# Kernel tuning notes

Measured on AMD Instinct MI355X. Metric: run time of the kernel, lower is better.

Reference implementation:

```python
import jax, jax.numpy as jnp
import numpy as np

B, T_MEL, T_TXT = 16, 2048, 1024
D_MODEL, D_ENC_M, D_ENC_T = 512, 512, 512
LN_EPS = 1e-5


def setup_inputs() -> dict:
    key = jax.random.key(0)
    ks = jax.random.split(key, 9)
    mel_encoding = jax.random.normal(ks[0], (B, T_MEL, D_ENC_M), dtype=jnp.float32)
    text_encoding = jax.random.normal(ks[1], (B, T_TXT, D_ENC_T), dtype=jnp.float32)
    mel_mask = jax.random.randint(ks[2], (B, T_MEL), 0, 2).astype(bool)
    mel_mask = mel_mask.at[:, 0].set(False)  # guarantee >=1 unmasked key per row
    src_mask = jax.random.randint(ks[3], (B, T_TXT), 0, 2).astype(bool)
    # Projection weights stored [in, out] (torch Linear does x @ W.T)
    sc = 1.0 / np.sqrt(D_ENC_M)
    Wq = jax.random.uniform(ks[4], (D_ENC_T, D_MODEL), jnp.float32, -sc, sc)
    Wk = jax.random.uniform(ks[5], (D_ENC_M, D_MODEL), jnp.float32, -sc, sc)
    Wv = jax.random.uniform(ks[6], (D_ENC_M, D_MODEL), jnp.float32, -sc, sc)
    ln_gamma = jnp.ones((D_MODEL,), jnp.float32)
    ln_beta = jnp.zeros((D_MODEL,), jnp.float32)
    return {"mel_encoding": mel_encoding, "text_encoding": text_encoding,
            "mel_mask": mel_mask, "src_mask": src_mask,
            "Wq": Wq, "Wk": Wk, "Wv": Wv,
            "ln_gamma": ln_gamma, "ln_beta": ln_beta}


def reference(mel_encoding, text_encoding, mel_mask, src_mask, Wq, Wk, Wv, ln_gamma, ln_beta):
    temperature = jnp.sqrt(jnp.float32(D_ENC_M))
    q = jnp.einsum('btd,dm->btm', text_encoding, Wq)   # [B, T_txt, d_model]
    k = jnp.einsum('bsd,dm->bsm', mel_encoding, Wk)    # [B, T_mel, d_model]
    v = jnp.einsum('bsd,dm->bsm', mel_encoding, Wv)
    # attn_mask = outer product of src_mask and mel_mask (True -> masked)
    attn_mask = src_mask[:, :, None] & mel_mask[:, None, :]  # [B, T_txt, T_mel]
    scores = jnp.einsum('btm,bsm->bts', q, k) / temperature
    scores = jnp.where(attn_mask, -jnp.inf, scores)
    attn = jax.nn.softmax(scores, axis=2)
    output = jnp.einsum('bts,bsm->btm', attn, v)
    # dropout is identity at inference; LayerNorm over last dim
    mean = jnp.mean(output, axis=-1, keepdims=True)
    var = jnp.var(output, axis=-1, keepdims=True)
    output = (output - mean) * jax.lax.rsqrt(var + LN_EPS) * ln_gamma + ln_beta
    return output, attn
```

## Files before the change

### kernel.cpp

```cpp
#include <hip/hip_runtime.h>

#define DEV __device__ __forceinline__

typedef __attribute__((ext_vector_type(8))) short short8v;
typedef __attribute__((ext_vector_type(4))) float f32x4;

DEV unsigned short f2bf(float f) {
  unsigned int x = __float_as_uint(f);
  x = x + 0x7FFFu + ((x >> 16) & 1u);
  return (unsigned short)(x >> 16);
}
DEV float bf2f(unsigned short u) {
  return __uint_as_float(((unsigned)u) << 16);
}

DEV int swz_byte(int row, int kElem) {
  int chunk = ((kElem >> 3) ^ (row & 7));
  return row * 128 + (chunk << 4) + ((kElem & 7) << 1);
}

template <int ROUNDS>
DEV void stage(const unsigned short* __restrict__ g, int ld,
               unsigned short* tile, int tid) {
  const int wave = tid >> 6, l = tid & 63;
#pragma unroll
  for (int p = 0; p < ROUNDS; ++p) {
    const int r = (p << 5) + (wave << 3) + (l >> 3);
    const int c = ((l & 7) ^ (r & 7)) << 3;
    const unsigned short* src = g + (long)r * ld + c;
#if __has_builtin(__builtin_amdgcn_global_load_lds)
    unsigned short* dst = tile + (p << 11) + (wave << 9);
    __builtin_amdgcn_global_load_lds(
        (const __attribute__((address_space(1))) void*)src,
        (__attribute__((address_space(3))) void*)dst, 16, 0, 0);
#else
    short8v v = *reinterpret_cast<const short8v*>(src);
    *reinterpret_cast<short8v*>(reinterpret_cast<char*>(tile) +
                                (p << 12) + (wave << 10) + (l << 4)) = v;
#endif
  }
}

template <int BM>
DEV void stage_f32(const float* __restrict__ g, int ld,
                   unsigned short* tile, int tid) {
  const int rl = tid >> 4;
  const int c4 = (tid & 15) << 2;
#pragma unroll
  for (int p = 0; p < BM / 16; ++p) {
    const int row = (p << 4) + rl;
    const float4 f = *reinterpret_cast<const float4*>(g + (long)row * ld + c4);
    ushort4 pack;
    pack.x = f2bf(f.x); pack.y = f2bf(f.y); pack.z = f2bf(f.z); pack.w = f2bf(f.w);
    *reinterpret_cast<ushort4*>(reinterpret_cast<char*>(tile) +
                                swz_byte(row, c4)) = pack;
  }
}

template <int BM, int EPI, int GM, bool AF32>
__global__ __launch_bounds__(256) void gemm_bf16(
    const void* __restrict__ Av, const unsigned short* __restrict__ B,
    void* __restrict__ Cout, int M, int N, int K,
    long aBatch, long bBatch, long cBatch,
    const int* __restrict__ srcMask, const int* __restrict__ melMask,
    float scale, float* __restrict__ stats) {
  constexpr int NI = BM / 32;
  __shared__ unsigned short As[BM * 64];
  __shared__ unsigned short Bs[128 * 64];
  const int tid = threadIdx.x;
  const int lane = tid & 63;
  const int wave = tid >> 6;
  int z, bmi, bni;
  if constexpr (GM == 1) {
    const int id = blockIdx.x;
    z = (id & 7) | ((id >> 10) << 3);
    const int ib = (id >> 3) & 127;
    bni = ib & 15;
    bmi = ib >> 4;
  } else if constexpr (GM == 2) {
    bmi = blockIdx.x; bni = blockIdx.y; z = blockIdx.z;
  } else {
    bni = blockIdx.x; bmi = blockIdx.y; z = blockIdx.z;
  }
  const int bm = bmi * BM;
  const int bn = bni * 128;
  const unsigned short* Bb = B + (long)z * bBatch;
  const long cOff = (long)z * cBatch;
  const int wr = (wave >> 1) * (BM / 2);
  const int wc = (wave & 1) * 64;
  const int l15 = lane & 15;
  const int lHi = lane >> 4;

  f32x4 acc[NI][4] = {};

  for (int kt = 0; kt < K; kt += 64) {
    if constexpr (AF32) {
      stage_f32<BM>((const float*)Av + (long)z * aBatch + (long)bm * K + kt, K, As, tid);
    } else {
      stage<BM / 32>((const unsigned short*)Av + (long)z * aBatch + (long)bm * K + kt,
                     K, As, tid);
    }
    stage<4>(Bb + (long)bn * K + kt, K, Bs, tid);
    __syncthreads();
#pragma unroll
    for (int ks = 0; ks < 2; ++ks) {
      const int k0 = (ks << 5) + (lHi << 3);
      short8v af[NI], bfr[4];
#pragma unroll
      for (int i = 0; i < NI; ++i)
        af[i] = *reinterpret_cast<const short8v*>(
            reinterpret_cast<const char*>(As) + swz_byte(wr + i * 16 + l15, k0));
#pragma unroll
      for (int j = 0; j < 4; ++j)
        bfr[j] = *reinterpret_cast<const short8v*>(
            reinterpret_cast<const char*>(Bs) + swz_byte(wc + j * 16 + l15, k0));
#pragma unroll
      for (int i = 0; i < NI; ++i)
#pragma unroll
        for (int j = 0; j < 4; ++j)
          acc[i][j] = __builtin_amdgcn_mfma_f32_16x16x32_bf16(af[i], bfr[j], acc[i][j], 0, 0, 0);
    }
    __syncthreads();
  }

  if constexpr (EPI == 2) {
    const int wcIdx = wave & 1;
#pragma unroll
    for (int i = 0; i < NI; ++i) {
#pragma unroll
      for (int rr = 0; rr < 4; ++rr) {
        const int rloc = wr + i * 16 + lHi * 4 + rr;
        const int rb = bm + rloc;
        const bool sm = srcMask[z * 1024 + rb] != 0;
        float vals[4];
        float m_l = -3.0e38f;
#pragma unroll
        for (int j = 0; j < 4; ++j) {
          const int c = bn + wc + j * 16 + l15;
          const bool mm = melMask[z * 2048 + c] != 0;
          const float vf = (sm && mm) ? -1e30f : acc[i][j][rr] * scale;
          vals[j] = vf;
          m_l = fmaxf(m_l, vf);
        }
#pragma unroll
        for (int o = 1; o < 16; o <<= 1) m_l = fmaxf(m_l, __shfl_xor(m_l, o, 64));
        float s_l = 0.f;
#pragma unroll
        for (int j = 0; j < 4; ++j) {
          const float pe = __expf(vals[j] - m_l);
          s_l += pe;
          const int c = bn + wc + j * 16 + l15;
          reinterpret_cast<unsigned short*>(Cout)[cOff + (long)rb * N + c] = f2bf(pe);
        }
#pragma unroll
        for (int o = 1; o < 16; o <<= 1) s_l += __shfl_xor(s_l, o, 64);
        if (l15 == 0) {
          const long sidx = ((long)(z * 1024 + rb)) * 64 + (long)(bni * 2 + wcIdx) * 2;
          stats[sidx] = m_l;
          stats[sidx + 1] = s_l;
        }
      }
    }
  } else {
#pragma unroll
    for (int i = 0; i < NI; ++i) {
#pragma unroll
      for (int j = 0; j < 4; ++j) {
        const int rb = bm + wr + i * 16 + lHi * 4;
        const int c = bn + wc + j * 16 + l15;
#pragma unroll
        for (int r = 0; r < 4; ++r) {
          const long idx = cOff + (long)(rb + r) * N + c;
          reinterpret_cast<unsigned short*>(Cout)[idx] = f2bf(acc[i][j][r]);
        }
      }
    }
  }
}

__global__ __launch_bounds__(256) void pv_smx(
    const unsigned short* __restrict__ sbf, const unsigned short* __restrict__ vT,
    float* __restrict__ attn, float* __restrict__ out,
    const float* __restrict__ stats) {
  __shared__ unsigned short As[2][64 * 64];
  __shared__ unsigned short Bs[2][128 * 64];
  __shared__ unsigned short scl[64][32];
  const int id = blockIdx.x;
  const int z = (id & 7) | ((id >> 9) << 3);
  const int ib = (id >> 3) & 63;
  const int mt = ib & 15, nt = ib >> 4;
  const int bm = mt * 64, bn = nt * 128;
  const int tid = threadIdx.x, lane = tid & 63, wave = tid >> 6;

  {
    const int row = tid >> 2;
    const float* st = stats + ((long)(z * 1024 + bm + row)) * 64;
    float Mx = -3.0e38f;
#pragma unroll
    for (int t = 0; t < 32; ++t) Mx = fmaxf(Mx, st[t * 2]);
    float S = 0.f;
#pragma unroll
    for (int t = 0; t < 32; ++t) S += st[t * 2 + 1] * __expf(st[t * 2] - Mx);
    const float inv = 1.0f / S;
    const int t0 = (tid & 3) * 8;
#pragma unroll
    for (int t = 0; t < 8; ++t)
      scl[row][t0 + t] = f2bf(__expf(st[(t0 + t) * 2] - Mx) * inv);
  }
  __syncthreads();

  const int ar = tid >> 2;
  const int ac = (tid & 3) << 4;
  const long aOff = ((long)z * 1024 + bm + ar) * 2048 + ac;
  const unsigned short* vTb = vT + ((long)z * 512 + bn) * 2048;
  const int wr = (wave >> 1) * 32, wc = (wave & 1) * 64;
  const int l15 = lane & 15, lHi = lane >> 4;

  f32x4 acc[2][4] = {};

  for (int it = 0; it < 16; ++it) {
    const int kt = it << 7;
    stage<4>(vTb + kt, 2048, Bs[0], tid);
    stage<4>(vTb + kt + 64, 2048, Bs[1], tid);
#pragma unroll
    for (int h = 0; h < 2; ++h) {
      const int kh = kt + (h << 6);
      const float sc = bf2f(scl[ar][kh >> 6]);
      const short8v s0 = *reinterpret_cast<const short8v*>(sbf + aOff + kh);
      const short8v s1 = *reinterpret_cast<const short8v*>(sbf + aOff + kh + 8);
      float e[16];
#pragma unroll
      for (int u = 0; u < 8; ++u) {
        e[u] = bf2f((unsigned short)s0[u]) * sc;
        e[u + 8] = bf2f((unsigned short)s1[u]) * sc;
      }
      if ((kh >> 9) == nt) {
        float* ap = attn + aOff + kh;
#pragma unroll
        for (int g = 0; g < 4; ++g) {
          float4 w;
          w.x = e[g * 4]; w.y = e[g * 4 + 1]; w.z = e[g * 4 + 2]; w.w = e[g * 4 + 3];
          *reinterpret_cast<float4*>(ap + g * 4) = w;
        }
      }
      short8v pk0, pk1;
#pragma unroll
      for (int u = 0; u < 8; ++u) {
        pk0[u] = (short)f2bf(e[u]);
        pk1[u] = (short)f2bf(e[u + 8]);
      }
      *reinterpret_cast<short8v*>(reinterpret_cast<char*>(As[h]) + swz_byte(ar, ac)) = pk0;
      *reinterpret_cast<short8v*>(reinterpret_cast<char*>(As[h]) + swz_byte(ar, ac + 8)) = pk1;
    }
    __syncthreads();

#pragma unroll
    for (int h = 0; h < 2; ++h) {
#pragma unroll
      for (int ks = 0; ks < 2; ++ks) {
        const int k0 = (ks << 5) + (lHi << 3);
        short8v af[2], bfr[4];
#pragma unroll
        for (int i = 0; i < 2; ++i)
          af[i] = *reinterpret_cast<const short8v*>(
              reinterpret_cast<const char*>(As[h]) + swz_byte(wr + i * 16 + l15, k0));
#pragma unroll
        for (int j = 0; j < 4; ++j)
          bfr[j] = *reinterpret_cast<const short8v*>(
              reinterpret_cast<const char*>(Bs[h]) + swz_byte(wc + j * 16 + l15, k0));
#pragma unroll
        for (int i = 0; i < 2; ++i)
#pragma unroll
          for (int j = 0; j < 4; ++j)
            acc[i][j] = __builtin_amdgcn_mfma_f32_16x16x32_bf16(af[i], bfr[j], acc[i][j], 0, 0, 0);
      }
    }
    __syncthreads();
  }

#pragma unroll
  for (int i = 0; i < 2; ++i)
#pragma unroll
    for (int j = 0; j < 4; ++j) {
      const int row = bm + wr + i * 16 + lHi * 4;
      const int col = bn + wc + j * 16 + l15;
#pragma unroll
      for (int rr = 0; rr < 4; ++rr)
        out[((long)z * 1024 + row + rr) * 512 + col] = acc[i][j][rr];
    }
}

__global__ __launch_bounds__(256) void f32_to_bf16(
    const float* __restrict__ in, unsigned short* __restrict__ out, long n) {
  long i = ((long)blockIdx.x * blockDim.x + threadIdx.x) * 8;
  const long stride = (long)gridDim.x * blockDim.x * 8;
  for (; i < n; i += stride) {
    const float4 a = *reinterpret_cast<const float4*>(in + i);
    const float4 b = *reinterpret_cast<const float4*>(in + i + 4);
    short8v o;
    o[0] = (short)f2bf(a.x); o[1] = (short)f2bf(a.y);
    o[2] = (short)f2bf(a.z); o[3] = (short)f2bf(a.w);
    o[4] = (short)f2bf(b.x); o[5] = (short)f2bf(b.y);
    o[6] = (short)f2bf(b.z); o[7] = (short)f2bf(b.w);
    *reinterpret_cast<short8v*>(out + i) = o;
  }
}

__global__ __launch_bounds__(256) void prep_w(
    const float* __restrict__ Wq, const float* __restrict__ Wk,
    const float* __restrict__ Wv, unsigned short* __restrict__ wqbf,
    unsigned short* __restrict__ wkbf, unsigned short* __restrict__ WvT) {
  const int zz = blockIdx.z;
  const int tx = threadIdx.x, ty = threadIdx.y;
  if (zz == 0) {
    __shared__ float t[32][33];
    const int bx = blockIdx.x * 32;
    const int by = blockIdx.y * 32;
#pragma unroll
    for (int i = 0; i < 4; ++i)
      t[ty + i * 8][tx] = Wv[(long)(by + ty + i * 8) * 512 + bx + tx];
    __syncthreads();
#pragma unroll
    for (int i = 0; i < 4; ++i)
      WvT[(long)(bx + ty + i * 8) * 512 + by + tx] = f2bf(t[tx][ty + i * 8]);
  } else {
    const float* in = (zz == 1) ? Wq : Wk;
    unsigned short* out = (zz == 1) ? wqbf : wkbf;
    const long base = ((long)(blockIdx.y * 16 + blockIdx.x) * 256 + ty * 32 + tx) * 4;
    const float4 f = *reinterpret_cast<const float4*>(in + base);
    ushort4 o;
    o.x = f2bf(f.x); o.y = f2bf(f.y); o.z = f2bf(f.z); o.w = f2bf(f.w);
    *reinterpret_cast<ushort4*>(out + base) = o;
  }
}

__global__ __launch_bounds__(64) void layernorm_rows(
    float* __restrict__ out, const float* __restrict__ gamma, const float* __restrict__ beta) {
  const long row = blockIdx.x;
  float4* p = reinterpret_cast<float4*>(out + row * 512);
  const int lane = threadIdx.x;
  float4 a = p[lane];
  float4 b = p[lane + 64];
  float s = ((a.x + a.y) + (a.z + a.w)) + ((b.x + b.y) + (b.z + b.w));
  float s2 = ((a.x * a.x + a.y * a.y) + (a.z * a.z + a.w * a.w)) +
             ((b.x * b.x + b.y * b.y) + (b.z * b.z + b.w * b.w));
#pragma unroll
  for (int o = 32; o; o >>= 1) {
    s += __shfl_xor(s, o, 64);
    s2 += __shfl_xor(s2, o, 64);
  }
  const float mean = s * (1.0f / 512.0f);
  const float var = s2 * (1.0f / 512.0f) - mean * mean;
  const float rstd = rsqrtf(var + 1e-5f);
  const float4 g0 = reinterpret_cast<const float4*>(gamma)[lane];
  const float4 g1 = reinterpret_cast<const float4*>(gamma)[lane + 64];
  const float4 c0 = reinterpret_cast<const float4*>(beta)[lane];
  const float4 c1 = reinterpret_cast<const float4*>(beta)[lane + 64];
  a.x = (a.x - mean) * rstd * g0.x + c0.x;
  a.y = (a.y - mean) * rstd * g0.y + c0.y;
  a.z = (a.z - mean) * rstd * g0.z + c0.z;
  a.w = (a.w - mean) * rstd * g0.w + c0.w;
  b.x = (b.x - mean) * rstd * g1.x + c1.x;
  b.y = (b.y - mean) * rstd * g1.y + c1.y;
  b.z = (b.z - mean) * rstd * g1.z + c1.z;
  b.w = (b.w - mean) * rstd * g1.w + c1.w;
  p[lane] = a;
  p[lane + 64] = b;
}

extern "C" void kernel_launch(void* const* d_in, const int* in_sizes, int n_in,
                              void* d_out, int out_size, void* d_ws, size_t ws_size,
                              hipStream_t stream) {
  const float* mel  = (const float*)d_in[0];
  const float* text = (const float*)d_in[1];
  const int* melMask = (const int*)d_in[2];
  const int* srcMask = (const int*)d_in[3];
  const float* Wq = (const float*)d_in[4];
  const float* Wk = (const float*)d_in[5];
  const float* Wv = (const float*)d_in[6];
  const float* gamma = (const float*)d_in[7];
  const float* beta  = (const float*)d_in[8];

  float* out = (float*)d_out;
  float* attn = (float*)d_out + (long)16 * 1024 * 512;

  unsigned short* ws = (unsigned short*)d_ws;
  unsigned short* wqbf = ws;
  unsigned short* wkbf = wqbf + 512 * 512;
  unsigned short* wvT  = wkbf + 512 * 512;
  unsigned short* Mt   = wvT + 512 * 512;
  unsigned short* melbf = Mt + 512 * 512;
  unsigned short* qbf  = melbf + (long)16 * 2048 * 512;
  unsigned short* vT   = qbf + (long)16 * 1024 * 512;
  unsigned short* sbf  = vT + (long)16 * 512 * 2048;
  float* stats = (float*)(sbf + (long)16 * 1024 * 2048);

  prep_w<<<dim3(16, 16, 3), dim3(32, 8), 0, stream>>>(Wq, Wk, Wv, wqbf, wkbf, wvT);
  f32_to_bf16<<<dim3(4096), 256, 0, stream>>>(mel, melbf, (long)16 * 2048 * 512);

  gemm_bf16<128, 0, 0, false><<<dim3(4, 4, 1), 256, 0, stream>>>(
      wkbf, wqbf, Mt, 512, 512, 512, 0, 0, 0, nullptr, nullptr, 1.0f, nullptr);
  gemm_bf16<128, 0, 2, true><<<dim3(128, 4, 1), 256, 0, stream>>>(
      text, Mt, qbf, 16384, 512, 512, 0, 0, 0, nullptr, nullptr, 1.0f, nullptr);
  gemm_bf16<128, 0, 0, false><<<dim3(16, 4, 16), 256, 0, stream>>>(
      wvT, melbf, vT, 512, 2048, 512, 0, (long)2048 * 512, (long)512 * 2048,
      nullptr, nullptr, 1.0f, nullptr);
  gemm_bf16<128, 2, 1, false><<<dim3(2048), 256, 0, stream>>>(
      qbf, melbf, sbf, 1024, 2048, 512,
      (long)1024 * 512, (long)2048 * 512, (long)1024 * 2048,
      srcMask, melMask, 0.044194173824159216f, stats);
  pv_smx<<<dim3(1024), 256, 0, stream>>>(sbf, vT, attn, out, stats);
  layernorm_rows<<<dim3(16 * 1024), 64, 0, stream>>>(out, gamma, beta);
}
```

Measured before the change: 259.3 us.

## Software-pipeline PV kernel with double-buffered K-steps and deferred nontemporal attn stores

Restructures the pv_smx main loop from 16 iterations of two 64-wide halves, with two barriers each, into 32 single-barrier steps. Each step stages and transforms the next K tile into the alternate buffer while the MFMAs consume the current one. Attention-probability writes are held in registers and flushed one step later using nontemporal stores, so global stores overlap compute and avoid polluting the cache. The scale table row is padded from 32 to 34 entries to reduce LDS bank conflicts. In exchange it carries extra registers for the pending values and relies on the single barrier to order the buffer reuse.

```diff
diff --git a/kernel.cpp b/kernel.cpp
--- a/kernel.cpp
+++ b/kernel.cpp
@@ -184,7 +184,7 @@
     const float* __restrict__ stats) {
   __shared__ unsigned short As[2][64 * 64];
   __shared__ unsigned short Bs[2][128 * 64];
-  __shared__ unsigned short scl[64][32];
+  __shared__ unsigned short scl[64][34];
   const int id = blockIdx.x;
   const int z = (id & 7) | ((id >> 9) << 3);
   const int ib = (id >> 3) & 63;
@@ -217,66 +217,80 @@
   const int l15 = lane & 15, lHi = lane >> 4;
 
   f32x4 acc[2][4] = {};
-
-  for (int it = 0; it < 16; ++it) {
-    const int kt = it << 7;
-    stage<4>(vTb + kt, 2048, Bs[0], tid);
-    stage<4>(vTb + kt + 64, 2048, Bs[1], tid);
-#pragma unroll
-    for (int h = 0; h < 2; ++h) {
-      const int kh = kt + (h << 6);
-      const float sc = bf2f(scl[ar][kh >> 6]);
-      const short8v s0 = *reinterpret_cast<const short8v*>(sbf + aOff + kh);
-      const short8v s1 = *reinterpret_cast<const short8v*>(sbf + aOff + kh + 8);
-      float e[16];
-#pragma unroll
-      for (int u = 0; u < 8; ++u) {
-        e[u] = bf2f((unsigned short)s0[u]) * sc;
-        e[u + 8] = bf2f((unsigned short)s1[u]) * sc;
+  float pend[16];
+  int pendKt = -1;
+
+  auto transform = [&](int t, unsigned short* AsB) {
+    const int kh = t << 6;
+    const float sc = bf2f(scl[ar][t]);
+    const short8v s0 = *reinterpret_cast<const short8v*>(sbf + aOff + kh);
+    const short8v s1 = *reinterpret_cast<const short8v*>(sbf + aOff + kh + 8);
+    float e[16];
+#pragma unroll
+    for (int u = 0; u < 8; ++u) {
+      e[u] = bf2f((unsigned short)s0[u]) * sc;
+      e[u + 8] = bf2f((unsigned short)s1[u]) * sc;
+    }
+    short8v pk0, pk1;
+#pragma unroll
+    for (int u = 0; u < 8; ++u) {
+      pk0[u] = (short)f2bf(e[u]);
+      pk1[u] = (short)f2bf(e[u + 8]);
+    }
+    *reinterpret_cast<short8v*>(reinterpret_cast<char*>(AsB) + swz_byte(ar, ac)) = pk0;
+    *reinterpret_cast<short8v*>(reinterpret_cast<char*>(AsB) + swz_byte(ar, ac + 8)) = pk1;
+    if ((kh >> 9) == nt) {
+#pragma unroll
+      for (int u = 0; u < 16; ++u) pend[u] = e[u];
+      pendKt = kh;
+    }
+  };
+  auto flushAttn = [&]() {
+    if (pendKt >= 0) {
+      float* ap = attn + aOff + pendKt;
+#pragma unroll
+      for (int g = 0; g < 4; ++g) {
+        f32x4 w;
+        w[0] = pend[g * 4]; w[1] = pend[g * 4 + 1];
+        w[2] = pend[g * 4 + 2]; w[3] = pend[g * 4 + 3];
+        __builtin_nontemporal_store(w, reinterpret_cast<f32x4*>(ap + g * 4));
       }
-      if ((kh >> 9) == nt) {
-        float* ap = attn + aOff + kh;
-#pragma unroll
-        for (int g = 0; g < 4; ++g) {
-          float4 w;
-          w.x = e[g * 4]; w.y = e[g * 4 + 1]; w.z = e[g * 4 + 2]; w.w = e[g * 4 + 3];
-          *reinterpret_cast<float4*>(ap + g * 4) = w;
-        }
-      }
-      short8v pk0, pk1;
-#pragma unroll
-      for (int u = 0; u < 8; ++u) {
-        pk0[u] = (short)f2bf(e[u]);
-        pk1[u] = (short)f2bf(e[u + 8]);
-      }
-      *reinterpret_cast<short8v*>(reinterpret_cast<char*>(As[h]) + swz_byte(ar, ac)) = pk0;
-      *reinterpret_cast<short8v*>(reinterpret_cast<char*>(As[h]) + swz_byte(ar, ac + 8)) = pk1;
+      pendKt = -1;
+    }
+  };
+
+  stage<4>(vTb, 2048, Bs[0], tid);
+  transform(0, As[0]);
+  __syncthreads();
+
+  for (int t = 0; t < 32; ++t) {
+    const int cur = t & 1, nxt = cur ^ 1;
+    flushAttn();
+    if (t < 31) {
+      stage<4>(vTb + ((t + 1) << 6), 2048, Bs[nxt], tid);
+      transform(t + 1, As[nxt]);
+    }
+#pragma unroll
+    for (int ks = 0; ks < 2; ++ks) {
+      const int k0 = (ks << 5) + (lHi << 3);
+      short8v af[2], bfr[4];
+#pragma unroll
+      for (int i = 0; i < 2; ++i)
+        af[i] = *reinterpret_cast<const short8v*>(
+            reinterpret_cast<const char*>(As[cur]) + swz_byte(wr + i * 16 + l15, k0));
+#pragma unroll
+      for (int j = 0; j < 4; ++j)
+        bfr[j] = *reinterpret_cast<const short8v*>(
+            reinterpret_cast<const char*>(Bs[cur]) + swz_byte(wc + j * 16 + l15, k0));
+#pragma unroll
+      for (int i = 0; i < 2; ++i)
+#pragma unroll
+        for (int j = 0; j < 4; ++j)
+          acc[i][j] = __builtin_amdgcn_mfma_f32_16x16x32_bf16(af[i], bfr[j], acc[i][j], 0, 0, 0);
     }
     __syncthreads();
-
-#pragma unroll
-    for (int h = 0; h < 2; ++h) {
-#pragma unroll
-      for (int ks = 0; ks < 2; ++ks) {
-        const int k0 = (ks << 5) + (lHi << 3);
-        short8v af[2], bfr[4];
-#pragma unroll
-        for (int i = 0; i < 2; ++i)
-          af[i] = *reinterpret_cast<const short8v*>(
-              reinterpret_cast<const char*>(As[h]) + swz_byte(wr + i * 16 + l15, k0));
-#pragma unroll
-        for (int j = 0; j < 4; ++j)
-          bfr[j] = *reinterpret_cast<const short8v*>(
-              reinterpret_cast<const char*>(Bs[h]) + swz_byte(wc + j * 16 + l15, k0));
-#pragma unroll
-        for (int i = 0; i < 2; ++i)
-#pragma unroll
-          for (int j = 0; j < 4; ++j)
-            acc[i][j] = __builtin_amdgcn_mfma_f32_16x16x32_bf16(af[i], bfr[j], acc[i][j], 0, 0, 0);
-      }
-    }
-    __syncthreads();
-  }
+  }
+  flushAttn();
 
 #pragma unroll
   for (int i = 0; i < 2; ++i)
```

Result: slower. 265.6 us (+2.5%).

## Fuse mel fp32-to-bf16 conversion into GEMM staging and enlarge PV tile

Applied to the files above, without the earlier changes.

Removes the standalone mel f32_to_bf16 pass and its bf16 buffer. The V-projection and QK^T GEMMs now read fp32 mel directly and convert it while staging B tiles into LDS. The pv_smx kernel moves from 64x128 tiles with a double-buffered 128-wide K step to 128x128 tiles with a 64-wide K step, halving the grid and increasing reuse of the V tiles. In exchange, mel is converted redundantly in two GEMMs and read from memory at twice the byte width. Using register staging for B instead of direct global-to-LDS loads may also slow the GEMM main loops.

```diff
diff --git a/kernel.cpp b/kernel.cpp
--- a/kernel.cpp
+++ b/kernel.cpp
@@ -41,13 +41,13 @@
   }
 }
 
-template <int BM>
+template <int R>
 DEV void stage_f32(const float* __restrict__ g, int ld,
                    unsigned short* tile, int tid) {
   const int rl = tid >> 4;
   const int c4 = (tid & 15) << 2;
 #pragma unroll
-  for (int p = 0; p < BM / 16; ++p) {
+  for (int p = 0; p < R / 16; ++p) {
     const int row = (p << 4) + rl;
     const float4 f = *reinterpret_cast<const float4*>(g + (long)row * ld + c4);
     ushort4 pack;
@@ -57,9 +57,9 @@
   }
 }
 
-template <int BM, int EPI, int GM, bool AF32>
+template <int BM, int EPI, int GM, bool AF32, bool BF32>
 __global__ __launch_bounds__(256) void gemm_bf16(
-    const void* __restrict__ Av, const unsigned short* __restrict__ B,
+    const void* __restrict__ Av, const void* __restrict__ Bv,
     void* __restrict__ Cout, int M, int N, int K,
     long aBatch, long bBatch, long cBatch,
     const int* __restrict__ srcMask, const int* __restrict__ melMask,
@@ -84,7 +84,6 @@
   }
   const int bm = bmi * BM;
   const int bn = bni * 128;
-  const unsigned short* Bb = B + (long)z * bBatch;
   const long cOff = (long)z * cBatch;
   const int wr = (wave >> 1) * (BM / 2);
   const int wc = (wave & 1) * 64;
@@ -100,7 +99,12 @@
       stage<BM / 32>((const unsigned short*)Av + (long)z * aBatch + (long)bm * K + kt,
                      K, As, tid);
     }
-    stage<4>(Bb + (long)bn * K + kt, K, Bs, tid);
+    if constexpr (BF32) {
+      stage_f32<128>((const float*)Bv + (long)z * bBatch + (long)bn * K + kt, K, Bs, tid);
+    } else {
+      stage<4>((const unsigned short*)Bv + (long)z * bBatch + (long)bn * K + kt,
+               K, Bs, tid);
+    }
     __syncthreads();
 #pragma unroll
     for (int ks = 0; ks < 2; ++ks) {
@@ -182,18 +186,18 @@
     const unsigned short* __restrict__ sbf, const unsigned short* __restrict__ vT,
     float* __restrict__ attn, float* __restrict__ out,
     const float* __restrict__ stats) {
-  __shared__ unsigned short As[2][64 * 64];
-  __shared__ unsigned short Bs[2][128 * 64];
-  __shared__ unsigned short scl[64][32];
+  __shared__ unsigned short As[128 * 64];
+  __shared__ unsigned short Bs[128 * 64];
+  __shared__ unsigned short scl[128][34];
   const int id = blockIdx.x;
-  const int z = (id & 7) | ((id >> 9) << 3);
-  const int ib = (id >> 3) & 63;
-  const int mt = ib & 15, nt = ib >> 4;
-  const int bm = mt * 64, bn = nt * 128;
+  const int z = (id & 7) | ((id >> 8) << 3);
+  const int ib = (id >> 3) & 31;
+  const int mt = ib & 7, nt = ib >> 3;
+  const int bm = mt * 128, bn = nt * 128;
   const int tid = threadIdx.x, lane = tid & 63, wave = tid >> 6;
 
   {
-    const int row = tid >> 2;
+    const int row = tid >> 1;
     const float* st = stats + ((long)(z * 1024 + bm + row)) * 64;
     float Mx = -3.0e38f;
 #pragma unroll
@@ -202,84 +206,78 @@
 #pragma unroll
     for (int t = 0; t < 32; ++t) S += st[t * 2 + 1] * __expf(st[t * 2] - Mx);
     const float inv = 1.0f / S;
-    const int t0 = (tid & 3) * 8;
-#pragma unroll
-    for (int t = 0; t < 8; ++t)
+    const int t0 = (tid & 1) * 16;
+#pragma unroll
+    for (int t = 0; t < 16; ++t)
       scl[row][t0 + t] = f2bf(__expf(st[(t0 + t) * 2] - Mx) * inv);
   }
   __syncthreads();
 
-  const int ar = tid >> 2;
-  const int ac = (tid & 3) << 4;
+  const int ar = tid >> 1;
+  const int ac = (tid & 1) << 5;
   const long aOff = ((long)z * 1024 + bm + ar) * 2048 + ac;
   const unsigned short* vTb = vT + ((long)z * 512 + bn) * 2048;
-  const int wr = (wave >> 1) * 32, wc = (wave & 1) * 64;
+  const int wr = (wave >> 1) * 64, wc = (wave & 1) * 64;
   const int l15 = lane & 15, lHi = lane >> 4;
 
-  f32x4 acc[2][4] = {};
-
-  for (int it = 0; it < 16; ++it) {
-    const int kt = it << 7;
-    stage<4>(vTb + kt, 2048, Bs[0], tid);
-    stage<4>(vTb + kt + 64, 2048, Bs[1], tid);
-#pragma unroll
-    for (int h = 0; h < 2; ++h) {
-      const int kh = kt + (h << 6);
-      const float sc = bf2f(scl[ar][kh >> 6]);
-      const short8v s0 = *reinterpret_cast<const short8v*>(sbf + aOff + kh);
-      const short8v s1 = *reinterpret_cast<const short8v*>(sbf + aOff + kh + 8);
-      float e[16];
-#pragma unroll
-      for (int u = 0; u < 8; ++u) {
-        e[u] = bf2f((unsigned short)s0[u]) * sc;
-        e[u + 8] = bf2f((unsigned short)s1[u]) * sc;
+  f32x4 acc[4][4] = {};
+
+  for (int t = 0; t < 32; ++t) {
+    const int kt = t << 6;
+    stage<4>(vTb + kt, 2048, Bs, tid);
+    const float sc = bf2f(scl[ar][t]);
+    short8v sv[4];
+#pragma unroll
+    for (int g = 0; g < 4; ++g)
+      sv[g] = *reinterpret_cast<const short8v*>(sbf + aOff + kt + g * 8);
+    float e[32];
+#pragma unroll
+    for (int g = 0; g < 4; ++g)
+#pragma unroll
+      for (int u = 0; u < 8; ++u)
+        e[g * 8 + u] = bf2f((unsigned short)sv[g][u]) * sc;
+    if ((kt >> 9) == nt) {
+      float* ap = attn + aOff + kt;
+#pragma unroll
+      for (int g = 0; g < 8; ++g) {
+        float4 w;
+        w.x = e[g * 4]; w.y = e[g * 4 + 1]; w.z = e[g * 4 + 2]; w.w = e[g * 4 + 3];
+        *reinterpret_cast<float4*>(ap + g * 4) = w;
       }
-      if ((kh >> 9) == nt) {
-        float* ap = attn + aOff + kh;
-#pragma unroll
-        for (int g = 0; g < 4; ++g) {
-          float4 w;
-          w.x = e[g * 4]; w.y = e[g * 4 + 1]; w.z = e[g * 4 + 2]; w.w = e[g * 4 + 3];
-          *reinterpret_cast<float4*>(ap + g * 4) = w;
-        }
-      }
-      short8v pk0, pk1;
-#pragma unroll
-      for (int u = 0; u < 8; ++u) {
-        pk0[u] = (short)f2bf(e[u]);
-        pk1[u] = (short)f2bf(e[u + 8]);
-      }
-      *reinterpret_cast<short8v*>(reinterpret_cast<char*>(As[h]) + swz_byte(ar, ac)) = pk0;
-      *reinterpret_cast<short8v*>(reinterpret_cast<char*>(As[h]) + swz_byte(ar, ac + 8)) = pk1;
-    }
-    __syncthreads();
-
-#pragma unroll
-    for (int h = 0; h < 2; ++h) {
-#pragma unroll
-      for (int ks = 0; ks < 2; ++ks) {
-        const int k0 = (ks << 5) + (lHi << 3);
-        short8v af[2], bfr[4];
-#pragma unroll
-        for (int i = 0; i < 2; ++i)
-          af[i] = *reinterpret_cast<const short8v*>(
-              reinterpret_cast<const char*>(As[h]) + swz_byte(wr + i * 16 + l15, k0));
+    }
+#pragma unroll
+    for (int g = 0; g < 4; ++g) {
+      short8v pk;
+#pragma unroll
+      for (int u = 0; u < 8; ++u) pk[u] = (short)f2bf(e[g * 8 + u]);
+      *reinterpret_cast<short8v*>(reinterpret_cast<char*>(As) +
+                                  swz_byte(ar, ac + g * 8)) = pk;
+    }
+    __syncthreads();
+
+#pragma unroll
+    for (int ks = 0; ks < 2; ++ks) {
+      const int k0 = (ks << 5) + (lHi << 3);
+      short8v af[4], bfr[4];
+#pragma unroll
+      for (int i = 0; i < 4; ++i)
+        af[i] = *reinterpret_cast<const short8v*>(
+            reinterpret_cast<const char*>(As) + swz_byte(wr + i * 16 + l15, k0));
+#pragma unroll
+      for (int j = 0; j < 4; ++j)
+        bfr[j] = *reinterpret_cast<const short8v*>(
+            reinterpret_cast<const char*>(Bs) + swz_byte(wc + j * 16 + l15, k0));
+#pragma unroll
+      for (int i = 0; i < 4; ++i)
 #pragma unroll
         for (int j = 0; j < 4; ++j)
-          bfr[j] = *reinterpret_cast<const short8v*>(
-              reinterpret_cast<const char*>(Bs[h]) + swz_byte(wc + j * 16 + l15, k0));
-#pragma unroll
-        for (int i = 0; i < 2; ++i)
-#pragma unroll
-          for (int j = 0; j < 4; ++j)
-            acc[i][j] = __builtin_amdgcn_mfma_f32_16x16x32_bf16(af[i], bfr[j], acc[i][j], 0, 0, 0);
-      }
-    }
-    __syncthreads();
-  }
-
-#pragma unroll
-  for (int i = 0; i < 2; ++i)
+          acc[i][j] = __builtin_amdgcn_mfma_f32_16x16x32_bf16(af[i], bfr[j], acc[i][j], 0, 0, 0);
+    }
+    __syncthreads();
+  }
+
+#pragma unroll
+  for (int i = 0; i < 4; ++i)
 #pragma unroll
     for (int j = 0; j < 4; ++j) {
       const int row = bm + wr + i * 16 + lHi * 4;
@@ -288,22 +286,6 @@
       for (int rr = 0; rr < 4; ++rr)
         out[((long)z * 1024 + row + rr) * 512 + col] = acc[i][j][rr];
     }
-}
-
-__global__ __launch_bounds__(256) void f32_to_bf16(
-    const float* __restrict__ in, unsigned short* __restrict__ out, long n) {
-  long i = ((long)blockIdx.x * blockDim.x + threadIdx.x) * 8;
-  const long stride = (long)gridDim.x * blockDim.x * 8;
-  for (; i < n; i += stride) {
-    const float4 a = *reinterpret_cast<const float4*>(in + i);
-    const float4 b = *reinterpret_cast<const float4*>(in + i + 4);
-    short8v o;
-    o[0] = (short)f2bf(a.x); o[1] = (short)f2bf(a.y);
-    o[2] = (short)f2bf(a.z); o[3] = (short)f2bf(a.w);
-    o[4] = (short)f2bf(b.x); o[5] = (short)f2bf(b.y);
-    o[6] = (short)f2bf(b.z); o[7] = (short)f2bf(b.w);
-    *reinterpret_cast<short8v*>(out + i) = o;
-  }
 }
 
 __global__ __launch_bounds__(256) void prep_w(
@@ -389,26 +371,24 @@
   unsigned short* wkbf = wqbf + 512 * 512;
   unsigned short* wvT  = wkbf + 512 * 512;
   unsigned short* Mt   = wvT + 512 * 512;
-  unsigned short* melbf = Mt + 512 * 512;
-  unsigned short* qbf  = melbf + (long)16 * 2048 * 512;
+  unsigned short* qbf  = Mt + 512 * 512;
   unsigned short* vT   = qbf + (long)16 * 1024 * 512;
   unsigned short* sbf  = vT + (long)16 * 512 * 2048;
   float* stats = (float*)(sbf + (long)16 * 1024 * 2048);
 
   prep_w<<<dim3(16, 16, 3), dim3(32, 8), 0, stream>>>(Wq, Wk, Wv, wqbf, wkbf, wvT);
-  f32_to_bf16<<<dim3(4096), 256, 0, stream>>>(mel, melbf, (long)16 * 2048 * 512);
-
-  gemm_bf16<128, 0, 0, false><<<dim3(4, 4, 1), 256, 0, stream>>>(
+
+  gemm_bf16<128, 0, 0, false, false><<<dim3(4, 4, 1), 256, 0, stream>>>(
       wkbf, wqbf, Mt, 512, 512, 512, 0, 0, 0, nullptr, nullptr, 1.0f, nullptr);
-  gemm_bf16<128, 0, 2, true><<<dim3(128, 4, 1), 256, 0, stream>>>(
+  gemm_bf16<128, 0, 2, true, false><<<dim3(128, 4, 1), 256, 0, stream>>>(
       text, Mt, qbf, 16384, 512, 512, 0, 0, 0, nullptr, nullptr, 1.0f, nullptr);
-  gemm_bf16<128, 0, 0, false><<<dim3(16, 4, 16), 256, 0, stream>>>(
-      wvT, melbf, vT, 512, 2048, 512, 0, (long)2048 * 512, (long)512 * 2048,
+  gemm_bf16<128, 0, 0, false, true><<<dim3(16, 4, 16), 256, 0, stream>>>(
+      wvT, mel, vT, 512, 2048, 512, 0, (long)2048 * 512, (long)512 * 2048,
       nullptr, nullptr, 1.0f, nullptr);
-  gemm_bf16<128, 2, 1, false><<<dim3(2048), 256, 0, stream>>>(
-      qbf, melbf, sbf, 1024, 2048, 512,
+  gemm_bf16<128, 2, 1, false, true><<<dim3(2048), 256, 0, stream>>>(
+      qbf, mel, sbf, 1024, 2048, 512,
       (long)1024 * 512, (long)2048 * 512, (long)1024 * 2048,
       srcMask, melMask, 0.044194173824159216f, stats);
-  pv_smx<<<dim3(1024), 256, 0, stream>>>(sbf, vT, attn, out, stats);
+  pv_smx<<<dim3(512), 256, 0, stream>>>(sbf, vT, attn, out, stats);
   layernorm_rows<<<dim3(16 * 1024), 64, 0, stream>>>(out, gamma, beta);
 }
```

Result: slower. 272.0 us (+4.9%).

## Software-pipeline PV GEMM with triple-buffered V tiles and hoisted attn writes

Applied to the files above, without the earlier changes.

Rewrites the pv_smx main loop as a 64-wide-K software pipeline. V tiles are triple-buffered in LDS and the next score tile is prefetched into registers while the current one is scaled and MFMAs run. A single barrier per step uses an explicit vmcnt wait, and MFMA sections get raised wave priority. The fp32 attention-probability store for the block's own column range moves into a separate prologue loop, so the hot loop no longer carries the conditional write. This adds LDS usage (a third B buffer and a padded scale array), which may reduce occupancy, and relies on hand-tuned waitcnt values being correct.

```diff
diff --git a/kernel.cpp b/kernel.cpp
--- a/kernel.cpp
+++ b/kernel.cpp
@@ -183,8 +183,8 @@
     float* __restrict__ attn, float* __restrict__ out,
     const float* __restrict__ stats) {
   __shared__ unsigned short As[2][64 * 64];
-  __shared__ unsigned short Bs[2][128 * 64];
-  __shared__ unsigned short scl[64][32];
+  __shared__ unsigned short Bs[3][128 * 64];
+  __shared__ unsigned short scl[64][34];
   const int id = blockIdx.x;
   const int z = (id & 7) | ((id >> 9) << 3);
   const int ib = (id >> 3) & 63;
@@ -216,67 +216,104 @@
   const int wr = (wave >> 1) * 32, wc = (wave & 1) * 64;
   const int l15 = lane & 15, lHi = lane >> 4;
 
+  {
+    const int row = tid >> 2;
+    const int c0 = (nt << 9) + ((tid & 3) << 7);
+    const unsigned short* sp = sbf + ((long)(z * 1024 + bm + row)) * 2048 + c0;
+    float* ap = attn + ((long)(z * 1024 + bm + row)) * 2048 + c0;
+#pragma unroll
+    for (int g = 0; g < 16; ++g) {
+      const float sc = bf2f(scl[row][(c0 + g * 8) >> 6]);
+      const short8v sv = *reinterpret_cast<const short8v*>(sp + g * 8);
+      float4 w0, w1;
+      w0.x = bf2f((unsigned short)sv[0]) * sc; w0.y = bf2f((unsigned short)sv[1]) * sc;
+      w0.z = bf2f((unsigned short)sv[2]) * sc; w0.w = bf2f((unsigned short)sv[3]) * sc;
+      w1.x = bf2f((unsigned short)sv[4]) * sc; w1.y = bf2f((unsigned short)sv[5]) * sc;
+      w1.z = bf2f((unsigned short)sv[6]) * sc; w1.w = bf2f((unsigned short)sv[7]) * sc;
+      *reinterpret_cast<float4*>(ap + g * 8) = w0;
+      *reinterpret_cast<float4*>(ap + g * 8 + 4) = w1;
+    }
+  }
+
   f32x4 acc[2][4] = {};
-
-  for (int it = 0; it < 16; ++it) {
-    const int kt = it << 7;
-    stage<4>(vTb + kt, 2048, Bs[0], tid);
-    stage<4>(vTb + kt + 64, 2048, Bs[1], tid);
-#pragma unroll
-    for (int h = 0; h < 2; ++h) {
-      const int kh = kt + (h << 6);
-      const float sc = bf2f(scl[ar][kh >> 6]);
-      const short8v s0 = *reinterpret_cast<const short8v*>(sbf + aOff + kh);
-      const short8v s1 = *reinterpret_cast<const short8v*>(sbf + aOff + kh + 8);
-      float e[16];
-#pragma unroll
-      for (int u = 0; u < 8; ++u) {
-        e[u] = bf2f((unsigned short)s0[u]) * sc;
-        e[u + 8] = bf2f((unsigned short)s1[u]) * sc;
-      }
-      if ((kh >> 9) == nt) {
-        float* ap = attn + aOff + kh;
-#pragma unroll
-        for (int g = 0; g < 4; ++g) {
-          float4 w;
-          w.x = e[g * 4]; w.y = e[g * 4 + 1]; w.z = e[g * 4 + 2]; w.w = e[g * 4 + 3];
-          *reinterpret_cast<float4*>(ap + g * 4) = w;
-        }
-      }
-      short8v pk0, pk1;
-#pragma unroll
-      for (int u = 0; u < 8; ++u) {
-        pk0[u] = (short)f2bf(e[u]);
-        pk1[u] = (short)f2bf(e[u + 8]);
-      }
-      *reinterpret_cast<short8v*>(reinterpret_cast<char*>(As[h]) + swz_byte(ar, ac)) = pk0;
-      *reinterpret_cast<short8v*>(reinterpret_cast<char*>(As[h]) + swz_byte(ar, ac + 8)) = pk1;
-    }
-    __syncthreads();
-
-#pragma unroll
-    for (int h = 0; h < 2; ++h) {
-#pragma unroll
-      for (int ks = 0; ks < 2; ++ks) {
-        const int k0 = (ks << 5) + (lHi << 3);
-        short8v af[2], bfr[4];
-#pragma unroll
-        for (int i = 0; i < 2; ++i)
-          af[i] = *reinterpret_cast<const short8v*>(
-              reinterpret_cast<const char*>(As[h]) + swz_byte(wr + i * 16 + l15, k0));
+  short8v s00, s01, s10, s11;
+  unsigned short* b0 = Bs[0];
+  unsigned short* b1 = Bs[1];
+  unsigned short* b2 = Bs[2];
+
+  auto transform = [&](int t, const short8v& t0, const short8v& t1,
+                       unsigned short* aWr) {
+    const float sc = bf2f(scl[ar][t]);
+    short8v pk0, pk1;
+#pragma unroll
+    for (int u = 0; u < 8; ++u) {
+      pk0[u] = (short)f2bf(bf2f((unsigned short)t0[u]) * sc);
+      pk1[u] = (short)f2bf(bf2f((unsigned short)t1[u]) * sc);
+    }
+    *reinterpret_cast<short8v*>(reinterpret_cast<char*>(aWr) + swz_byte(ar, ac)) = pk0;
+    *reinterpret_cast<short8v*>(reinterpret_cast<char*>(aWr) + swz_byte(ar, ac + 8)) = pk1;
+  };
+  auto mfma_step = [&](const unsigned short* aRd, const unsigned short* bRd) {
+    __builtin_amdgcn_s_setprio(1);
+#pragma unroll
+    for (int ks = 0; ks < 2; ++ks) {
+      const int k0 = (ks << 5) + (lHi << 3);
+      short8v af[2], bfr[4];
+#pragma unroll
+      for (int i = 0; i < 2; ++i)
+        af[i] = *reinterpret_cast<const short8v*>(
+            reinterpret_cast<const char*>(aRd) + swz_byte(wr + i * 16 + l15, k0));
+#pragma unroll
+      for (int j = 0; j < 4; ++j)
+        bfr[j] = *reinterpret_cast<const short8v*>(
+            reinterpret_cast<const char*>(bRd) + swz_byte(wc + j * 16 + l15, k0));
+#pragma unroll
+      for (int i = 0; i < 2; ++i)
 #pragma unroll
         for (int j = 0; j < 4; ++j)
-          bfr[j] = *reinterpret_cast<const short8v*>(
-              reinterpret_cast<const char*>(Bs[h]) + swz_byte(wc + j * 16 + l15, k0));
-#pragma unroll
-        for (int i = 0; i < 2; ++i)
-#pragma unroll
-          for (int j = 0; j < 4; ++j)
-            acc[i][j] = __builtin_amdgcn_mfma_f32_16x16x32_bf16(af[i], bfr[j], acc[i][j], 0, 0, 0);
-      }
-    }
-    __syncthreads();
-  }
+          acc[i][j] = __builtin_amdgcn_mfma_f32_16x16x32_bf16(af[i], bfr[j], acc[i][j], 0, 0, 0);
+    }
+    __builtin_amdgcn_s_setprio(0);
+  };
+
+  stage<4>(vTb, 2048, b0, tid);
+  s00 = *reinterpret_cast<const short8v*>(sbf + aOff);
+  s01 = *reinterpret_cast<const short8v*>(sbf + aOff + 8);
+  stage<4>(vTb + 64, 2048, b1, tid);
+  s10 = *reinterpret_cast<const short8v*>(sbf + aOff + 64);
+  s11 = *reinterpret_cast<const short8v*>(sbf + aOff + 72);
+  transform(0, s00, s01, As[0]);
+  asm volatile("s_waitcnt vmcnt(6) lgkmcnt(0)" ::: "memory");
+  __builtin_amdgcn_s_barrier();
+  __builtin_amdgcn_sched_barrier(0);
+
+#define PV_BODY(T, LD0, LD1, TF0, TF1, AWR, ARD)                               \
+  {                                                                            \
+    stage<4>(vTb + (((T) + 2) << 6), 2048, b2, tid);                           \
+    LD0 = *reinterpret_cast<const short8v*>(sbf + aOff + (((T) + 2) << 6));    \
+    LD1 = *reinterpret_cast<const short8v*>(sbf + aOff + (((T) + 2) << 6) + 8);\
+    transform((T) + 1, TF0, TF1, AWR);                                         \
+    mfma_step(ARD, b0);                                                        \
+    asm volatile("s_waitcnt vmcnt(6) lgkmcnt(0)" ::: "memory");                \
+    __builtin_amdgcn_s_barrier();                                              \
+    __builtin_amdgcn_sched_barrier(0);                                         \
+    unsigned short* btmp = b0; b0 = b1; b1 = b2; b2 = btmp;                    \
+  }
+
+  for (int i = 0; i < 15; ++i) {
+    const int t = 2 * i;
+    PV_BODY(t,     s00, s01, s10, s11, As[1], As[0]);
+    PV_BODY(t + 1, s10, s11, s00, s01, As[0], As[1]);
+  }
+#undef PV_BODY
+
+  transform(31, s10, s11, As[1]);
+  mfma_step(As[0], b0);
+  asm volatile("s_waitcnt vmcnt(0) lgkmcnt(0)" ::: "memory");
+  __builtin_amdgcn_s_barrier();
+  __builtin_amdgcn_sched_barrier(0);
+  { unsigned short* btmp = b0; b0 = b1; b1 = b2; b2 = btmp; }
+  mfma_step(As[1], b0);
 
 #pragma unroll
   for (int i = 0; i < 2; ++i)
```

After: 303.1 us. 1.17x slower.
